# Kernel tuning notes

Hardware: AMD Instinct MI355X
Metric: run time of the kernel (lower is better)

Reference implementation:

```python
import jax, jax.numpy as jnp
import numpy as np
from jax import lax

B, C, HW = 8, 512, 32
NH = 8            # num_heads
NG = 32           # num_groups
HD = C // NH      # head_size = 64
EPS = 1e-6


def group_norm(x, gamma, beta, groups=NG, eps=EPS):
    b, c, h, w = x.shape
    xr = x.reshape(b, groups, c // groups, h, w)
    mu = xr.mean(axis=(2, 3, 4), keepdims=True)
    var = xr.var(axis=(2, 3, 4), keepdims=True)
    xn = ((xr - mu) / jnp.sqrt(var + eps)).reshape(b, c, h, w)
    return xn * gamma[None, :, None, None] + beta[None, :, None, None]


def conv2d(x, w, b):
    y = lax.conv_general_dilated(x, w, (1, 1), 'SAME',
                                 dimension_numbers=('NCHW', 'OIHW', 'NCHW'))
    return y + b[None, :, None, None]


def setup_inputs() -> dict:
    key = jax.random.key(0)
    ks = jax.random.split(key, 24)
    f32 = jnp.float32

    def lin(k, out_d, in_d):
        return (jax.random.normal(k, (out_d, in_d), f32) / np.sqrt(in_d)).astype(f32)

    inp = {
        'hidden_states': jax.random.normal(ks[0], (B, C, HW, HW), f32),
        'pre_g': jnp.ones(C, f32), 'pre_b': jnp.zeros(C, f32),
        'norm_g': jnp.ones(C, f32), 'norm_b': jnp.zeros(C, f32),
        'post_g': jnp.ones(C, f32), 'post_b': jnp.zeros(C, f32),
        'pos_emb': jax.random.normal(ks[1], (1, C, 32, 32), f32) * 0.02,
        'sa_w1': (jax.random.normal(ks[2], (C // 8, C, 1, 1), f32) / np.sqrt(C)),
        'sa_b1': jnp.zeros(C // 8, f32),
        'sa_w2': (jax.random.normal(ks[3], (C // 8, C // 8, 3, 3), f32) / np.sqrt(9 * C // 8)),
        'sa_b2': jnp.zeros(C // 8, f32),
        'sa_w3': (jax.random.normal(ks[4], (1, C // 8, 1, 1), f32) / np.sqrt(C // 8)),
        'sa_b3': jnp.zeros(1, f32),
        'wq': lin(ks[5], C, C), 'wk': lin(ks[6], C, C), 'wv': lin(ks[7], C, C),
        'wq0': lin(ks[8], C // 2, C), 'wk0': lin(ks[9], C // 2, C), 'wv0': lin(ks[10], C // 2, C),
        'wq1': lin(ks[11], C // 2, C), 'wk1': lin(ks[12], C // 2, C), 'wv1': lin(ks[13], C // 2, C),
        'ff_w1': lin(ks[14], C, 2 * C), 'ff_b1': jnp.zeros(C, f32),
        'ff_w2': lin(ks[15], C, C), 'ff_b2': jnp.zeros(C, f32),
        'out_w': lin(ks[16], C, C), 'out_b': jnp.zeros(C, f32),
    }
    return inp


def reference(hidden_states, pre_g, pre_b, norm_g, norm_b, post_g, post_b,
              pos_emb, sa_w1, sa_b1, sa_w2, sa_b2, sa_w3, sa_b3,
              wq, wk, wv, wq0, wk0, wv0, wq1, wk1, wv1,
              ff_w1, ff_b1, ff_w2, ff_b2, out_w, out_b):
    b, c, h, w = hidden_states.shape
    S = h * w
    residual = hidden_states

    hs = group_norm(hidden_states, pre_g, pre_b)
    # H=W=32 matches pos_embedding; bilinear resize to same size is identity
    hs = hs + pos_emb

    # spatial attention gating (conv 1x1 -> SiLU -> conv 3x3 -> SiLU -> conv 1x1 -> sigmoid)
    a = jax.nn.silu(conv2d(hs, sa_w1, sa_b1))
    a = jax.nn.silu(conv2d(a, sa_w2, sa_b2))
    spatial_weights = jax.nn.sigmoid(conv2d(a, sa_w3, sa_b3))
    spatial_enhanced = hs * spatial_weights

    # standard multi-head self-attention over flattened tokens
    sh = group_norm(hs, norm_g, norm_b).reshape(b, c, S).transpose(0, 2, 1)  # (B,S,C)
    ehs = sh  # encoder_hidden_states defaults to standard_hidden

    q = (sh @ wq.T).reshape(b, S, NH, HD)
    k = (ehs @ wk.T).reshape(b, S, NH, HD)
    v = (ehs @ wv.T).reshape(b, S, NH, HD)
    scores = jnp.einsum('bqhd,bkhd->bhqk', q, k) / np.sqrt(HD)
    probs = jax.nn.softmax(scores, axis=-1)
    std_out = jnp.einsum('bhqk,bkhd->bqhd', probs, v).reshape(b, S, c)

    # two multi-scale single-head attention branches (dim C/2 each)
    msh = spatial_enhanced.reshape(b, c, S).transpose(0, 2, 1)  # (B,S,C)
    parts = []
    for wqm, wkm, wvm in ((wq0, wk0, wv0), (wq1, wk1, wv1)):
        qm = msh @ wqm.T          # (B,S,C/2)
        km = ehs @ wkm.T
        vm = ehs @ wvm.T
        sc = jnp.einsum('bqd,bkd->bqk', qm, km) / np.sqrt(c // 2)
        parts.append(jnp.einsum('bqk,bkd->bqd', jax.nn.softmax(sc, axis=-1), vm))
    multi_out = jnp.concatenate(parts, axis=-1)  # (B,S,C)

    combined = jnp.concatenate([std_out, multi_out], axis=-1)  # (B,S,2C)
    fused = jax.nn.silu(combined @ ff_w1.T + ff_b1) @ ff_w2.T + ff_b2  # dropout = eval identity
    final = fused @ out_w.T + out_b
    final = final.transpose(0, 2, 1).reshape(b, c, h, w)
    final = group_norm(final, post_g, post_b)
    return final + residual
```

## Files before the change

kernel.cpp:

```cpp
#include <hip/hip_runtime.h>
#include <hip/hip_bf16.h>
#include <math.h>

typedef __attribute__((ext_vector_type(8))) __bf16 v8bf;
typedef __attribute__((ext_vector_type(4))) float v4f;

__device__ __forceinline__ unsigned short f2bf(float f) {
  union { float f; unsigned int u; } a; a.f = f;
  unsigned int r = a.u + 0x7fffu + ((a.u >> 16) & 1u);
  return (unsigned short)(r >> 16);
}
__device__ __forceinline__ unsigned short f2bf_trunc(float f) {
  union { float f; unsigned int u; } a; a.f = f;
  return (unsigned short)(a.u >> 16);
}
__device__ __forceinline__ float bf2f(unsigned short u) {
  union { unsigned int i; float f; } a; a.i = ((unsigned int)u) << 16; return a.f;
}
__device__ __forceinline__ float sigm(float x) { return 1.0f / (1.0f + __expf(-x)); }

__device__ __forceinline__ void async16(const void* g, void* l) {
  __builtin_amdgcn_global_load_lds(
      (const __attribute__((address_space(1))) unsigned int*)g,
      (__attribute__((address_space(3))) unsigned int*)l, 16, 0, 0);
}

__global__ __launch_bounds__(256) void gn_pre_kernel(
    const float* __restrict__ x, const float* __restrict__ g, const float* __restrict__ be,
    const float* __restrict__ pos, unsigned short* __restrict__ hsb, float* __restrict__ stats) {
  __shared__ float L[16384];
  __shared__ float rs[4], rs2[4], mr[2];
  int b = blockIdx.x >> 5, grp = blockIdx.x & 31;
  const float4* base = (const float4*)(x + ((size_t)b*512 + grp*16)*1024);
  float4* L4 = (float4*)L;
  int w = threadIdx.x >> 6;
  float s = 0.f, s2 = 0.f;
  for (int i = threadIdx.x; i < 4096; i += 256) {
    float4 v = base[i];
    L4[i] = v;
    s += v.x + v.y + v.z + v.w;
    s2 += v.x*v.x + v.y*v.y + v.z*v.z + v.w*v.w;
  }
#pragma unroll
  for (int o = 32; o; o >>= 1) { s += __shfl_xor(s, o); s2 += __shfl_xor(s2, o); }
  if ((threadIdx.x & 63) == 0) { rs[w] = s; rs2[w] = s2; }
  __syncthreads();
  if (threadIdx.x == 0) {
    float ts = rs[0]+rs[1]+rs[2]+rs[3], ts2 = rs2[0]+rs2[1]+rs2[2]+rs2[3];
    float mu = ts * (1.0f/16384.0f);
    float var = ts2 * (1.0f/16384.0f) - mu*mu;
    mr[0] = mu; mr[1] = rsqrtf(var + 1e-6f);
  }
  __syncthreads();
  float mu = mr[0], rstd = mr[1];
  const float4* pb = (const float4*)(pos + (size_t)grp*16*1024);
  float ns = 0.f, ns2 = 0.f;
  for (int i = threadIdx.x; i < 4096; i += 256) {
    float4 v = L4[i], p = pb[i];
    int c = grp*16 + (i >> 8);
    float gg = g[c], bb = be[c];
    float4 o;
    o.x = (v.x - mu)*rstd*gg + bb + p.x;
    o.y = (v.y - mu)*rstd*gg + bb + p.y;
    o.z = (v.z - mu)*rstd*gg + bb + p.z;
    o.w = (v.w - mu)*rstd*gg + bb + p.w;
    L4[i] = o;
    ns += o.x + o.y + o.z + o.w;
    ns2 += o.x*o.x + o.y*o.y + o.z*o.z + o.w*o.w;
  }
#pragma unroll
  for (int o = 32; o; o >>= 1) { ns += __shfl_xor(ns, o); ns2 += __shfl_xor(ns2, o); }
  if ((threadIdx.x & 63) == 0) { rs[w] = ns; rs2[w] = ns2; }
  __syncthreads();
  if (threadIdx.x == 0) {
    float ts = rs[0]+rs[1]+rs[2]+rs[3], ts2 = rs2[0]+rs2[1]+rs2[2]+rs2[3];
    float nmu = ts * (1.0f/16384.0f);
    float nvar = ts2 * (1.0f/16384.0f) - nmu*nmu;
    stats[(b*32+grp)*2] = nmu; stats[(b*32+grp)*2+1] = rsqrtf(nvar + 1e-6f);
  }
#pragma unroll
  for (int j = 0; j < 4; ++j) {
    int sI = threadIdx.x + j*256;
    unsigned int wd[8];
#pragma unroll
    for (int c = 0; c < 8; ++c) {
      unsigned int lo = f2bf(L[(2*c)*1024 + sI]);
      unsigned int hi = f2bf(L[(2*c+1)*1024 + sI]);
      wd[c] = lo | (hi << 16);
    }
    size_t oo = (size_t)(b*1024 + sI)*512 + grp*16;
    *(uint4*)(hsb + oo)     = make_uint4(wd[0], wd[1], wd[2], wd[3]);
    *(uint4*)(hsb + oo + 8) = make_uint4(wd[4], wd[5], wd[6], wd[7]);
  }
}

__global__ __launch_bounds__(256) void im2col_kernel(
    const unsigned short* __restrict__ a1, unsigned short* __restrict__ im2) {
  int row0 = blockIdx.x * 8;
#pragma unroll
  for (int it = 0; it < 3; ++it) {
    int cc = it*256 + threadIdx.x;
    if (cc >= 576) break;
    int rl = cc / 72, rr = cc - rl*72;
    int tap = rr >> 3, ch8 = rr & 7;
    int row = row0 + rl;
    int bb = row >> 10, s = row & 1023;
    int y = s >> 5, xx0 = s & 31;
    int yy = y + tap/3 - 1, xx = xx0 + tap%3 - 1;
    ushort4 v0 = make_ushort4(0,0,0,0), v1 = make_ushort4(0,0,0,0);
    if ((unsigned)yy < 32u && (unsigned)xx < 32u) {
      const unsigned short* src = a1 + ((size_t)(bb*1024 + yy*32 + xx))*64 + ch8*8;
      v0 = *(const ushort4*)src; v1 = *(const ushort4*)(src + 4);
    }
    unsigned short* dst = im2 + (size_t)row*576 + tap*64 + ch8*8;
    *(ushort4*)dst = v0; *(ushort4*)(dst + 4) = v1;
  }
}

__global__ __launch_bounds__(256) void gate_norm_kernel(
    const unsigned short* __restrict__ hsb, const unsigned short* __restrict__ a2,
    const float* __restrict__ w3, const float* __restrict__ b3,
    const float* __restrict__ stats, const float* __restrict__ g,
    const float* __restrict__ be,
    unsigned short* __restrict__ sh, unsigned short* __restrict__ msh) {
  int b = blockIdx.y;
  int s = blockIdx.x * 4 + (threadIdx.x >> 6);
  int oct = threadIdx.x & 63;
  int c0 = oct * 8;
  int grp = c0 >> 4;
  float part = bf2f(a2[((size_t)(b*1024) + s)*64 + oct]) * w3[oct];
#pragma unroll
  for (int o = 32; o; o >>= 1) part += __shfl_xor(part, o);
  float wgt = sigm(part + b3[0]);
  float mu = stats[(b*32 + grp)*2], rstd = stats[(b*32 + grp)*2 + 1];
  size_t o = (size_t)(b*1024 + s)*512 + c0;
  ushort4 u0 = *(const ushort4*)(hsb + o), u1 = *(const ushort4*)(hsb + o + 4);
  unsigned short uu[8] = {u0.x,u0.y,u0.z,u0.w,u1.x,u1.y,u1.z,u1.w};
  unsigned short so[8], mo[8];
#pragma unroll
  for (int j = 0; j < 8; ++j) {
    float v = bf2f(uu[j]);
    so[j] = f2bf((v - mu)*rstd*g[c0+j] + be[c0+j]);
    mo[j] = f2bf(v * wgt);
  }
  *(ushort4*)(sh + o)     = make_ushort4(so[0], so[1], so[2], so[3]);
  *(ushort4*)(sh + o + 4) = make_ushort4(so[4], so[5], so[6], so[7]);
  *(ushort4*)(msh + o)     = make_ushort4(mo[0], mo[1], mo[2], mo[3]);
  *(ushort4*)(msh + o + 4) = make_ushort4(mo[4], mo[5], mo[6], mo[7]);
}

struct WCvt { const float* src; int dstOff; int n; float scale; };
struct WCvtArgs { WCvt w[15]; };
__global__ __launch_bounds__(256) void wconvert_kernel(WCvtArgs a, unsigned short* __restrict__ dst) {
  WCvt e = a.w[blockIdx.y];
  int i = blockIdx.x * 256 + threadIdx.x;
  if (i >= e.n) return;
  if (blockIdx.y == 13) {
    int oc = i / 576, r = i - oc*576;
    int tap = r >> 6, ic = r & 63;
    dst[e.dstOff + i] = f2bf(e.src[(oc*64 + ic)*9 + tap]);
  } else if (blockIdx.y == 14) {
    dst[e.dstOff + i] = f2bf(e.src[(i & 511)*512 + (i >> 9)]);
  } else {
    dst[e.dstOff + i] = f2bf(e.src[i] * e.scale);
  }
}

__global__ __launch_bounds__(256) void bias_fold_kernel(
    const float* __restrict__ ow, const float* __restrict__ b2,
    const float* __restrict__ ob, float* __restrict__ bc) {
  int n = blockIdx.x * 256 + threadIdx.x;
  float s = ob[n];
  const float* r = ow + (size_t)n * 512;
#pragma unroll 8
  for (int j = 0; j < 512; ++j) s += r[j] * b2[j];
  bc[n] = s;
}

__global__ __launch_bounds__(256) void transpose2_kernel(
    const unsigned short* __restrict__ qkvm,
    unsigned short* __restrict__ vtb, unsigned short* __restrict__ vmt) {
  __shared__ unsigned short t[64][65];
  int s0 = blockIdx.x * 64, c0 = blockIdx.y * 64;
  int z = blockIdx.z, b = z & 7;
  const unsigned short* in = qkvm + (z >= 8 ? 2048 : 1024);
  unsigned short* out = (z >= 8) ? vmt : vtb;
  int tx = threadIdx.x & 63, ty = threadIdx.x >> 6;
#pragma unroll
  for (int i = 0; i < 16; ++i) {
    int s = ty + i*4;
    t[s][tx] = in[((size_t)(b*1024 + s0 + s))*2560 + c0 + tx];
  }
  __syncthreads();
#pragma unroll
  for (int i = 0; i < 16; ++i) {
    int c = ty + i*4;
    out[((size_t)b*512 + c0 + c)*1024 + s0 + tx] = t[tx][c];
  }
}

struct GemmDesc {
  const unsigned short* A; const unsigned short* B; void* out; const float* bias;
  int M, N, K, lda, ldb, ldo, epi;
  long long Ay, Az, By, Bz, Oy, Oz;
};

template<int BM, int BN>
__global__ __launch_bounds__(256) void gemm_tile_kernel(GemmDesc d) {
  constexpr int WGM = (BN >= 128) ? 2 : 4;
  constexpr int WGN = 4 / WGM;
  constexpr int MT = BM / (16 * WGM);
  constexpr int NT = BN / (16 * WGN);
  constexpr int AIT = (BM * 4) / 256;
  constexpr int BIT = (BN * 4) / 256;
  __shared__ __align__(16) unsigned short As[BM * 32];
  __shared__ __align__(16) unsigned short Bs[BN * 32];

  int ntx = d.N / BN, mtx = d.M / BM;
  int bmt, bnt;
  if ((mtx & 7) == 0) {
    int xcd = blockIdx.x & 7, j = blockIdx.x >> 3;
    int mpx = mtx >> 3;
    bmt = xcd * mpx + (j % mpx);
    bnt = j / mpx;
  } else {
    bmt = blockIdx.x / ntx; bnt = blockIdx.x % ntx;
  }
  int bm0 = bmt * BM, bn0 = bnt * BN;
  const unsigned short* A = d.A + (long long)blockIdx.y * d.Ay
      + (long long)blockIdx.z * d.Az + (size_t)bm0 * d.lda;
  const unsigned short* B = d.B + (long long)blockIdx.y * d.By
      + (long long)blockIdx.z * d.Bz + (size_t)bn0 * d.ldb;
  int tid = threadIdx.x, lane = tid & 63, w = tid >> 6;
  int wm = (WGN == 2) ? (w >> 1) : w;
  int wn = (WGN == 2) ? (w & 1) : 0;
  int ln = lane & 15, qd = lane >> 4;

  v4f acc[MT][NT];
#pragma unroll
  for (int i = 0; i < MT; ++i)
#pragma unroll
    for (int j = 0; j < NT; ++j) acc[i][j] = (v4f){0.f, 0.f, 0.f, 0.f};

  int nks = d.K >> 5;
  for (int ks = 0; ks < nks; ++ks) {
    int kof = ks * 32;
#pragma unroll
    for (int it = 0; it < AIT; ++it) {
      int c = it * 256 + tid;
      async16(A + (size_t)(c >> 2) * d.lda + (c & 3) * 8 + kof,
              As + (it * 256 + w * 64) * 8);
    }
#pragma unroll
    for (int it = 0; it < BIT; ++it) {
      int c = it * 256 + tid;
      async16(B + (size_t)(c >> 2) * d.ldb + (c & 3) * 8 + kof,
              Bs + (it * 256 + w * 64) * 8);
    }
    __syncthreads();
    v8bf af[MT], bfr[NT];
#pragma unroll
    for (int i = 0; i < MT; ++i)
      af[i] = *(const v8bf*)(As + (wm * MT * 16 + i * 16 + ln) * 32 + qd * 8);
#pragma unroll
    for (int j = 0; j < NT; ++j)
      bfr[j] = *(const v8bf*)(Bs + (wn * NT * 16 + j * 16 + ln) * 32 + qd * 8);
#pragma unroll
    for (int i = 0; i < MT; ++i)
#pragma unroll
      for (int j = 0; j < NT; ++j)
        acc[i][j] = __builtin_amdgcn_mfma_f32_16x16x32_bf16(af[i], bfr[j], acc[i][j], 0, 0, 0);
    __syncthreads();
  }

  size_t obase = (size_t)((long long)blockIdx.y * d.Oy + (long long)blockIdx.z * d.Oz);
#pragma unroll
  for (int i = 0; i < MT; ++i) {
#pragma unroll
    for (int j = 0; j < NT; ++j) {
      int col = bn0 + wn * NT * 16 + j * 16 + ln;
      float bia = d.bias ? d.bias[col] : 0.0f;
#pragma unroll
      for (int r = 0; r < 4; ++r) {
        int row = bm0 + wm * MT * 16 + i * 16 + qd * 4 + r;
        float v = acc[i][j][r] + bia;
        if (d.epi == 2) v = v * sigm(v);
        size_t oi = obase + (size_t)row * d.ldo + col;
        if (d.epi == 0) ((float*)d.out)[oi] = v;
        else ((unsigned short*)d.out)[oi] = f2bf(v);
      }
    }
  }
}

__global__ __launch_bounds__(256) void flash_attn_kernel(
    const unsigned short* __restrict__ QKVM, const unsigned short* __restrict__ VTB,
    unsigned short* __restrict__ out) {
  __shared__ __align__(16) unsigned short Ks[128*64];
  __shared__ __align__(16) unsigned short Vts[64*128];
  __shared__ __align__(16) unsigned short Pw[4][16*128];
  int h = blockIdx.x, b = blockIdx.y, qt = blockIdx.z;
  int tid = threadIdx.x, lane = tid & 63, w = tid >> 6;
  int ln = lane & 15, qd = lane >> 4;

  const unsigned short* Qbase = QKVM + ((size_t)(b*1024 + qt*128 + w*32))*2560 + h*64;
  v8bf aq[2][2];
#pragma unroll
  for (int i = 0; i < 2; ++i)
#pragma unroll
    for (int s = 0; s < 2; ++s)
      aq[i][s] = *(const v8bf*)(Qbase + (size_t)(i*16 + ln)*2560 + s*32 + qd*8);

  v4f o_acc[2][4];
  float l_part[2][4];
#pragma unroll
  for (int i = 0; i < 2; ++i)
#pragma unroll
    for (int dn = 0; dn < 4; ++dn) o_acc[i][dn] = (v4f){0.f,0.f,0.f,0.f};
#pragma unroll
  for (int i = 0; i < 2; ++i)
#pragma unroll
    for (int r = 0; r < 4; ++r) l_part[i][r] = 0.f;

  const unsigned short* Kg = QKVM + 512 + (size_t)(b*1024)*2560 + h*64;
  const unsigned short* Vg = VTB + ((size_t)(b*512) + h*64)*1024;

  for (int kt = 0; kt < 8; ++kt) {
#pragma unroll
    for (int it = 0; it < 4; ++it) {
      int c = it*256 + tid;
      async16(Kg + (size_t)(kt*128 + (c >> 3))*2560 + (((c & 7) ^ ((c >> 3) & 7)) << 3),
              Ks + c*8);
    }
#pragma unroll
    for (int it = 0; it < 4; ++it) {
      int c = it*256 + tid;
      async16(Vg + (size_t)(c >> 4)*1024 + kt*128 + ((((c & 15) ^ ((c >> 4) & 7))) << 3),
              Vts + c*8);
    }
    __syncthreads();

#pragma unroll
    for (int i = 0; i < 2; ++i) {
      v4f sc[8];
#pragma unroll
      for (int n = 0; n < 8; ++n) {
        v4f a = (v4f){0.f,0.f,0.f,0.f};
#pragma unroll
        for (int s = 0; s < 2; ++s) {
          v8bf kb = *(const v8bf*)(Ks + (n*16 + ln)*64 + (((s*4 + qd) ^ (ln & 7)) << 3));
          a = __builtin_amdgcn_mfma_f32_16x16x32_bf16(aq[i][s], kb, a, 0, 0, 0);
        }
        sc[n] = a;
      }
#pragma unroll
      for (int r = 0; r < 4; ++r) {
        int row7 = (qd*4 + r) & 7;
        float acc_l = 0.f;
#pragma unroll
        for (int n = 0; n < 8; ++n) {
          float p = exp2f(sc[n][r]);
          acc_l += p;
          Pw[w][(qd*4 + r)*128 + (((n*2 + (ln >> 3)) ^ row7) << 3) + (ln & 7)] = f2bf_trunc(p);
        }
        l_part[i][r] += acc_l;
      }
#pragma unroll
      for (int dn = 0; dn < 4; ++dn) {
        v4f a = o_acc[i][dn];
#pragma unroll
        for (int ks2 = 0; ks2 < 4; ++ks2) {
          int phys = (((ks2*4 + qd) ^ (ln & 7)) << 3);
          v8bf pf = *(const v8bf*)(&Pw[w][ln*128 + phys]);
          v8bf vf = *(const v8bf*)(Vts + (dn*16 + ln)*128 + phys);
          a = __builtin_amdgcn_mfma_f32_16x16x32_bf16(pf, vf, a, 0, 0, 0);
        }
        o_acc[i][dn] = a;
      }
    }
    __syncthreads();
  }

  unsigned short* ob = out + ((size_t)(b*1024 + qt*128 + w*32))*1024 + h*64;
#pragma unroll
  for (int i = 0; i < 2; ++i)
#pragma unroll
    for (int r = 0; r < 4; ++r) {
      float l = l_part[i][r];
      l += __shfl_xor(l, 1); l += __shfl_xor(l, 2);
      l += __shfl_xor(l, 4); l += __shfl_xor(l, 8);
      float rinv = 1.0f / l;
#pragma unroll
      for (int dn = 0; dn < 4; ++dn)
        ob[(size_t)(i*16 + qd*4 + r)*1024 + dn*16 + ln] = f2bf(o_acc[i][dn][r] * rinv);
    }
}

__global__ __launch_bounds__(256) void softmax_bf16_kernel(
    const unsigned short* __restrict__ S, unsigned short* __restrict__ P, int nrows) {
  int row = blockIdx.x * 4 + (threadIdx.x >> 6);
  if (row >= nrows) return;
  int l = threadIdx.x & 63;
  const ushort4* sp = (const ushort4*)(S + (size_t)row * 1024);
  float v[16];
  float m = -1e30f;
#pragma unroll
  for (int t = 0; t < 4; ++t) {
    ushort4 u = sp[t*64 + l];
    v[t*4+0] = bf2f(u.x); v[t*4+1] = bf2f(u.y); v[t*4+2] = bf2f(u.z); v[t*4+3] = bf2f(u.w);
    m = fmaxf(m, fmaxf(fmaxf(v[t*4], v[t*4+1]), fmaxf(v[t*4+2], v[t*4+3])));
  }
#pragma unroll
  for (int o = 32; o; o >>= 1) m = fmaxf(m, __shfl_xor(m, o));
  float sum = 0.f;
#pragma unroll
  for (int t = 0; t < 16; ++t) { v[t] = __expf(v[t] - m); sum += v[t]; }
#pragma unroll
  for (int o = 32; o; o >>= 1) sum += __shfl_xor(sum, o);
  float r = 1.0f / sum;
  ushort4* p = (ushort4*)(P + (size_t)row * 1024);
#pragma unroll
  for (int t = 0; t < 4; ++t)
    p[t*64 + l] = make_ushort4(f2bf_trunc(v[t*4]*r), f2bf_trunc(v[t*4+1]*r),
                               f2bf_trunc(v[t*4+2]*r), f2bf_trunc(v[t*4+3]*r));
}

__global__ __launch_bounds__(256) void gn_stats_bf16_kernel(
    const unsigned short* __restrict__ t, float* __restrict__ stats) {
  int b = blockIdx.x >> 5, grp = blockIdx.x & 31;
  float s = 0.f, s2 = 0.f;
#pragma unroll
  for (int j = 0; j < 4; ++j) {
    int sI = threadIdx.x + j*256;
    const unsigned short* p = t + ((size_t)(b*1024 + sI))*512 + grp*16;
    uint4 a = *(const uint4*)p, c2 = *(const uint4*)(p + 8);
    unsigned int ww[8] = {a.x,a.y,a.z,a.w,c2.x,c2.y,c2.z,c2.w};
#pragma unroll
    for (int k = 0; k < 8; ++k) {
      float lo = bf2f((unsigned short)(ww[k] & 0xffff));
      float hi = bf2f((unsigned short)(ww[k] >> 16));
      s += lo + hi; s2 += lo*lo + hi*hi;
    }
  }
#pragma unroll
  for (int o = 32; o; o >>= 1) { s += __shfl_xor(s, o); s2 += __shfl_xor(s2, o); }
  __shared__ float rs[4], rs2[4];
  int w = threadIdx.x >> 6;
  if ((threadIdx.x & 63) == 0) { rs[w] = s; rs2[w] = s2; }
  __syncthreads();
  if (threadIdx.x == 0) {
    float ts = rs[0]+rs[1]+rs[2]+rs[3], ts2 = rs2[0]+rs2[1]+rs2[2]+rs2[3];
    float mu = ts * (1.0f/16384.0f);
    float var = ts2 * (1.0f/16384.0f) - mu*mu;
    stats[(b*32+grp)*2] = mu; stats[(b*32+grp)*2+1] = rsqrtf(var + 1e-6f);
  }
}

__global__ __launch_bounds__(256) void final_out_kernel(
    const unsigned short* __restrict__ fin, const float* __restrict__ stats,
    const float* __restrict__ g, const float* __restrict__ be,
    const float* __restrict__ x, float* __restrict__ out) {
  __shared__ float t[64][65];
  int s0 = blockIdx.x * 64, c0 = blockIdx.y * 64, b = blockIdx.z;
  int tx = threadIdx.x & 63, ty = threadIdx.x >> 6;
#pragma unroll
  for (int i = 0; i < 16; ++i) {
    int s = ty + i*4;
    t[s][tx] = bf2f(fin[((size_t)(b*1024 + s0 + s))*512 + c0 + tx]);
  }
  __syncthreads();
#pragma unroll
  for (int i = 0; i < 16; ++i) {
    int c = ty + i*4;
    int cc = c0 + c, grp = cc >> 4;
    float mu = stats[(b*32+grp)*2], rstd = stats[(b*32+grp)*2+1];
    float gg = g[cc], bb = be[cc];
    size_t oi = ((size_t)(b*512 + cc))*1024 + s0 + tx;
    out[oi] = (t[tx][c] - mu)*rstd*gg + bb + x[oi];
  }
}

static void launch_gemm128(hipStream_t st, const unsigned short* A, const unsigned short* B,
                           void* out, const float* bias,
                           int M, int N, int K, int lda, int ldb, int ldo, int epi,
                           long long Ay, long long Az, long long By, long long Bz,
                           long long Oy, long long Oz, int gy, int gz) {
  GemmDesc d{A, B, out, bias, M, N, K, lda, ldb, ldo, epi, Ay, Az, By, Bz, Oy, Oz};
  gemm_tile_kernel<128,128><<<dim3((M/128)*(N/128), gy, gz), dim3(256), 0, st>>>(d);
}
static void launch_gemm64(hipStream_t st, const unsigned short* A, const unsigned short* B,
                          void* out, const float* bias,
                          int M, int N, int K, int lda, int ldb, int ldo, int epi) {
  GemmDesc d{A, B, out, bias, M, N, K, lda, ldb, ldo, epi, 0,0,0,0,0,0};
  gemm_tile_kernel<128,64><<<dim3((M/128)*(N/64), 1, 1), dim3(256), 0, st>>>(d);
}

extern "C" void kernel_launch(void* const* d_in, const int* in_sizes, int n_in,
                              void* d_out, int out_size, void* d_ws, size_t ws_size,
                              hipStream_t stream) {
  const float* x      = (const float*)d_in[0];
  const float* pre_g  = (const float*)d_in[1];
  const float* pre_b  = (const float*)d_in[2];
  const float* norm_g = (const float*)d_in[3];
  const float* norm_b = (const float*)d_in[4];
  const float* post_g = (const float*)d_in[5];
  const float* post_b = (const float*)d_in[6];
  const float* pos    = (const float*)d_in[7];
  const float* sa_b1  = (const float*)d_in[9];
  const float* sa_b2  = (const float*)d_in[11];
  const float* sa_w3  = (const float*)d_in[12];
  const float* sa_b3  = (const float*)d_in[13];
  const float* ff_b1  = (const float*)d_in[24];
  const float* ff_b2  = (const float*)d_in[26];
  const float* out_w  = (const float*)d_in[27];
  const float* out_b  = (const float*)d_in[28];
  float* outp = (float*)d_out;

  char* ws = (char*)d_ws;
  size_t off = 0;
  auto alloc = [&](size_t bytes) -> void* {
    void* p = ws + off; off += (bytes + 255) & ~(size_t)255; return p;
  };
  float* STATS = (float*)alloc(4096);
  float* BC    = (float*)alloc(2048);
  unsigned short* HSB  = (unsigned short*)alloc(8388608);
  unsigned short* A1   = (unsigned short*)alloc(1048576);
  unsigned short* IM2  = (unsigned short*)alloc(9437184);
  unsigned short* A2   = (unsigned short*)alloc(1048576);
  unsigned short* SHB  = (unsigned short*)alloc(8388608);
  unsigned short* MSHB = (unsigned short*)alloc(8388608);
  unsigned short* WBF  = (unsigned short*)alloc(6291456);
  unsigned short* WCOMB= (unsigned short*)alloc(524288);
  unsigned short* QKVM = (unsigned short*)alloc(41943040);
  unsigned short* QM   = (unsigned short*)alloc(8388608);
  unsigned short* VTB  = (unsigned short*)alloc(8388608);
  unsigned short* VMT  = (unsigned short*)alloc(8388608);
  unsigned short* SBUF = (unsigned short*)alloc(33554432);
  unsigned short* PBUF = (unsigned short*)alloc(33554432);
  unsigned short* COMB = (unsigned short*)alloc(16777216);
  unsigned short* FFMID= (unsigned short*)alloc(8388608);
  unsigned short* FINALB=(unsigned short*)alloc(8388608);

  const int OQKVM=0, OQM=1310720, OFF1=1572864, OFF2T=2097152,
            OOW=2359296, OW1=2621440, OW2R=2654208;

  gn_pre_kernel<<<dim3(256), dim3(256), 0, stream>>>(x, pre_g, pre_b, pos, HSB, STATS);
  {
    WCvtArgs a;
    const float LG2E = 1.4426950408889634f;
    const int   srcIdx[15] = {14,15,16, 18,21,19,22, 17,20, 23,27, 8, 0 , 10, 25};
    const int   dofs[15]   = {0, 262144, 524288,
                              786432, 917504, 1048576, 1179648,
                              OQM, OQM+131072,
                              OFF1, OOW, OW1, 0, OW2R, OFF2T};
    const int   ns[15]     = {262144,262144,262144, 131072,131072,131072,131072,
                              131072,131072, 524288,262144, 32768, 0, 36864, 262144};
    const float sc[15]     = {0.125f*LG2E,1.f,1.f, 1.f,1.f,1.f,1.f,
                              0.0625f,0.0625f, 1.f,1.f, 1.f, 0.f, 1.f, 1.f};
    for (int i = 0; i < 15; ++i) { a.w[i].src = (const float*)d_in[srcIdx[i]]; a.w[i].dstOff = dofs[i]; a.w[i].n = ns[i]; a.w[i].scale = sc[i]; }
    wconvert_kernel<<<dim3(2048, 15), dim3(256), 0, stream>>>(a, WBF);
  }
  {
    GemmDesc d{WBF+OOW, WBF+OFF2T, WCOMB, nullptr, 512, 512, 512, 512, 512, 512, 1, 0,0,0,0,0,0};
    gemm_tile_kernel<128,128><<<dim3(16, 1, 1), dim3(256), 0, stream>>>(d);
  }
  bias_fold_kernel<<<dim3(2), dim3(256), 0, stream>>>(out_w, ff_b2, out_b, BC);
  launch_gemm64(stream, HSB, WBF+OW1,  A1, sa_b1, 8192, 64, 512, 512, 512, 64, 2);
  im2col_kernel<<<dim3(1024), dim3(256), 0, stream>>>(A1, IM2);
  launch_gemm64(stream, IM2, WBF+OW2R, A2, sa_b2, 8192, 64, 576, 576, 576, 64, 2);
  gate_norm_kernel<<<dim3(256, 8), dim3(256), 0, stream>>>(HSB, A2, sa_w3, sa_b3, STATS, norm_g, norm_b, SHB, MSHB);

  launch_gemm128(stream, SHB,  WBF+OQKVM, QKVM, nullptr, 8192, 2560, 512, 512, 512, 2560, 1, 0,0,0,0,0,0, 1,1);
  launch_gemm128(stream, MSHB, WBF+OQM,   QM,   nullptr, 8192, 512,  512, 512, 512, 512,  1, 0,0,0,0,0,0, 1,1);

  transpose2_kernel<<<dim3(16, 8, 16), dim3(256), 0, stream>>>(QKVM, VTB, VMT);

  flash_attn_kernel<<<dim3(8, 8, 8), dim3(256), 0, stream>>>(QKVM, VTB, COMB);

  launch_gemm128(stream, QM, QKVM + 1536, SBUF, nullptr,
                 1024, 1024, 256, 512, 2560, 1024, 1,
                 1024LL*512, 256, 1024LL*2560, 256, 1024LL*1024, 8388608, 8, 2);
  softmax_bf16_kernel<<<dim3(4096), dim3(256), 0, stream>>>(SBUF, PBUF, 16384);
  launch_gemm128(stream, PBUF, VMT, COMB + 512, nullptr,
                 1024, 256, 1024, 1024, 1024, 1024, 1,
                 1024LL*1024, 8388608, 512LL*1024, 256LL*1024, 1024LL*1024, 256, 8, 2);

  launch_gemm128(stream, COMB,  WBF+OFF1, FFMID,  ff_b1, 8192, 512, 1024, 1024, 1024, 512, 2, 0,0,0,0,0,0, 1,1);
  launch_gemm128(stream, FFMID, WCOMB,    FINALB, BC,    8192, 512, 512,  512,  512,  512, 1, 0,0,0,0,0,0, 1,1);

  gn_stats_bf16_kernel<<<dim3(256), dim3(256), 0, stream>>>(FINALB, STATS);
  final_out_kernel<<<dim3(16, 8, 8), dim3(256), 0, stream>>>(FINALB, STATS, post_g, post_b, x, outp);

  (void)in_sizes; (void)n_in; (void)out_size; (void)ws_size;
}
```

Measured before the change: 457.3 us.

## Deepen GEMM K-tile with swizzled LDS, widen flash-attn blocks, use smaller GEMM tiles

The generic GEMM now stages a 64-wide K slice per iteration with an XOR-swizzled LDS layout. This halves the barriers per K step and is meant to cut LDS bank conflicts, at the cost of twice the shared memory per block. Flash attention moves to 512-thread blocks, each wave holding 16 query rows instead of 32, so K/V tiles in LDS are shared across more waves and per-wave register use drops. Three N=512 GEMMs switch to the 64-wide tile launcher to put more blocks on the GPU.

```diff
diff --git a/kernel.cpp b/kernel.cpp
--- a/kernel.cpp
+++ b/kernel.cpp
@@ -211,10 +211,10 @@
   constexpr int WGN = 4 / WGM;
   constexpr int MT = BM / (16 * WGM);
   constexpr int NT = BN / (16 * WGN);
-  constexpr int AIT = (BM * 4) / 256;
-  constexpr int BIT = (BN * 4) / 256;
-  __shared__ __align__(16) unsigned short As[BM * 32];
-  __shared__ __align__(16) unsigned short Bs[BN * 32];
+  constexpr int AIT = (BM * 8) / 256;
+  constexpr int BIT = (BN * 8) / 256;
+  __shared__ __align__(16) unsigned short As[BM * 64];
+  __shared__ __align__(16) unsigned short Bs[BN * 64];
 
   int ntx = d.N / BN, mtx = d.M / BM;
   int bmt, bnt;
@@ -242,34 +242,41 @@
 #pragma unroll
     for (int j = 0; j < NT; ++j) acc[i][j] = (v4f){0.f, 0.f, 0.f, 0.f};
 
-  int nks = d.K >> 5;
+  int nks = d.K >> 6;
   for (int ks = 0; ks < nks; ++ks) {
-    int kof = ks * 32;
+    int kof = ks * 64;
 #pragma unroll
     for (int it = 0; it < AIT; ++it) {
       int c = it * 256 + tid;
-      async16(A + (size_t)(c >> 2) * d.lda + (c & 3) * 8 + kof,
-              As + (it * 256 + w * 64) * 8);
+      int row = c >> 3, ch = c & 7;
+      async16(A + (size_t)row * d.lda + ((ch ^ (row & 7)) << 3) + kof, As + c * 8);
     }
 #pragma unroll
     for (int it = 0; it < BIT; ++it) {
       int c = it * 256 + tid;
-      async16(B + (size_t)(c >> 2) * d.ldb + (c & 3) * 8 + kof,
-              Bs + (it * 256 + w * 64) * 8);
+      int row = c >> 3, ch = c & 7;
+      async16(B + (size_t)row * d.ldb + ((ch ^ (row & 7)) << 3) + kof, Bs + c * 8);
     }
     __syncthreads();
-    v8bf af[MT], bfr[NT];
-#pragma unroll
-    for (int i = 0; i < MT; ++i)
-      af[i] = *(const v8bf*)(As + (wm * MT * 16 + i * 16 + ln) * 32 + qd * 8);
-#pragma unroll
-    for (int j = 0; j < NT; ++j)
-      bfr[j] = *(const v8bf*)(Bs + (wn * NT * 16 + j * 16 + ln) * 32 + qd * 8);
-#pragma unroll
-    for (int i = 0; i < MT; ++i)
-#pragma unroll
-      for (int j = 0; j < NT; ++j)
-        acc[i][j] = __builtin_amdgcn_mfma_f32_16x16x32_bf16(af[i], bfr[j], acc[i][j], 0, 0, 0);
+#pragma unroll
+    for (int k2 = 0; k2 < 2; ++k2) {
+      v8bf af[MT], bfr[NT];
+#pragma unroll
+      for (int i = 0; i < MT; ++i) {
+        int row = wm * MT * 16 + i * 16 + ln;
+        af[i] = *(const v8bf*)(As + row * 64 + (((k2*4 + qd) ^ (ln & 7)) << 3));
+      }
+#pragma unroll
+      for (int j = 0; j < NT; ++j) {
+        int row = wn * NT * 16 + j * 16 + ln;
+        bfr[j] = *(const v8bf*)(Bs + row * 64 + (((k2*4 + qd) ^ (ln & 7)) << 3));
+      }
+#pragma unroll
+      for (int i = 0; i < MT; ++i)
+#pragma unroll
+        for (int j = 0; j < NT; ++j)
+          acc[i][j] = __builtin_amdgcn_mfma_f32_16x16x32_bf16(af[i], bfr[j], acc[i][j], 0, 0, 0);
+    }
     __syncthreads();
   }
 
@@ -293,107 +300,96 @@
   }
 }
 
-__global__ __launch_bounds__(256) void flash_attn_kernel(
+__global__ __launch_bounds__(512) void flash_attn_kernel(
     const unsigned short* __restrict__ QKVM, const unsigned short* __restrict__ VTB,
     unsigned short* __restrict__ out) {
   __shared__ __align__(16) unsigned short Ks[128*64];
   __shared__ __align__(16) unsigned short Vts[64*128];
-  __shared__ __align__(16) unsigned short Pw[4][16*128];
+  __shared__ __align__(16) unsigned short Pw[8][16*128];
   int h = blockIdx.x, b = blockIdx.y, qt = blockIdx.z;
   int tid = threadIdx.x, lane = tid & 63, w = tid >> 6;
   int ln = lane & 15, qd = lane >> 4;
 
-  const unsigned short* Qbase = QKVM + ((size_t)(b*1024 + qt*128 + w*32))*2560 + h*64;
-  v8bf aq[2][2];
-#pragma unroll
-  for (int i = 0; i < 2; ++i)
-#pragma unroll
-    for (int s = 0; s < 2; ++s)
-      aq[i][s] = *(const v8bf*)(Qbase + (size_t)(i*16 + ln)*2560 + s*32 + qd*8);
-
-  v4f o_acc[2][4];
-  float l_part[2][4];
-#pragma unroll
-  for (int i = 0; i < 2; ++i)
-#pragma unroll
-    for (int dn = 0; dn < 4; ++dn) o_acc[i][dn] = (v4f){0.f,0.f,0.f,0.f};
-#pragma unroll
-  for (int i = 0; i < 2; ++i)
-#pragma unroll
-    for (int r = 0; r < 4; ++r) l_part[i][r] = 0.f;
+  const unsigned short* Qbase = QKVM + ((size_t)(b*1024 + qt*128 + w*16))*2560 + h*64;
+  v8bf aq[2];
+#pragma unroll
+  for (int s = 0; s < 2; ++s)
+    aq[s] = *(const v8bf*)(Qbase + (size_t)ln*2560 + s*32 + qd*8);
+
+  v4f o_acc[4];
+  float l_part[4];
+#pragma unroll
+  for (int dn = 0; dn < 4; ++dn) o_acc[dn] = (v4f){0.f,0.f,0.f,0.f};
+#pragma unroll
+  for (int r = 0; r < 4; ++r) l_part[r] = 0.f;
 
   const unsigned short* Kg = QKVM + 512 + (size_t)(b*1024)*2560 + h*64;
   const unsigned short* Vg = VTB + ((size_t)(b*512) + h*64)*1024;
 
   for (int kt = 0; kt < 8; ++kt) {
 #pragma unroll
-    for (int it = 0; it < 4; ++it) {
-      int c = it*256 + tid;
+    for (int it = 0; it < 2; ++it) {
+      int c = it*512 + tid;
       async16(Kg + (size_t)(kt*128 + (c >> 3))*2560 + (((c & 7) ^ ((c >> 3) & 7)) << 3),
               Ks + c*8);
     }
 #pragma unroll
-    for (int it = 0; it < 4; ++it) {
-      int c = it*256 + tid;
+    for (int it = 0; it < 2; ++it) {
+      int c = it*512 + tid;
       async16(Vg + (size_t)(c >> 4)*1024 + kt*128 + ((((c & 15) ^ ((c >> 4) & 7))) << 3),
               Vts + c*8);
     }
     __syncthreads();
 
-#pragma unroll
-    for (int i = 0; i < 2; ++i) {
-      v4f sc[8];
+    v4f sc[8];
+#pragma unroll
+    for (int n = 0; n < 8; ++n) {
+      v4f a = (v4f){0.f,0.f,0.f,0.f};
+#pragma unroll
+      for (int s = 0; s < 2; ++s) {
+        v8bf kb = *(const v8bf*)(Ks + (n*16 + ln)*64 + (((s*4 + qd) ^ (ln & 7)) << 3));
+        a = __builtin_amdgcn_mfma_f32_16x16x32_bf16(aq[s], kb, a, 0, 0, 0);
+      }
+      sc[n] = a;
+    }
+#pragma unroll
+    for (int r = 0; r < 4; ++r) {
+      int row7 = (qd*4 + r) & 7;
+      float acc_l = 0.f;
 #pragma unroll
       for (int n = 0; n < 8; ++n) {
-        v4f a = (v4f){0.f,0.f,0.f,0.f};
-#pragma unroll
-        for (int s = 0; s < 2; ++s) {
-          v8bf kb = *(const v8bf*)(Ks + (n*16 + ln)*64 + (((s*4 + qd) ^ (ln & 7)) << 3));
-          a = __builtin_amdgcn_mfma_f32_16x16x32_bf16(aq[i][s], kb, a, 0, 0, 0);
-        }
-        sc[n] = a;
+        float p = exp2f(sc[n][r]);
+        acc_l += p;
+        Pw[w][(qd*4 + r)*128 + (((n*2 + (ln >> 3)) ^ row7) << 3) + (ln & 7)] = f2bf_trunc(p);
       }
-#pragma unroll
-      for (int r = 0; r < 4; ++r) {
-        int row7 = (qd*4 + r) & 7;
-        float acc_l = 0.f;
-#pragma unroll
-        for (int n = 0; n < 8; ++n) {
-          float p = exp2f(sc[n][r]);
-          acc_l += p;
-          Pw[w][(qd*4 + r)*128 + (((n*2 + (ln >> 3)) ^ row7) << 3) + (ln & 7)] = f2bf_trunc(p);
-        }
-        l_part[i][r] += acc_l;
+      l_part[r] += acc_l;
+    }
+#pragma unroll
+    for (int dn = 0; dn < 4; ++dn) {
+      v4f a = o_acc[dn];
+#pragma unroll
+      for (int ks2 = 0; ks2 < 4; ++ks2) {
+        int phys = (((ks2*4 + qd) ^ (ln & 7)) << 3);
+        v8bf pf = *(const v8bf*)(&Pw[w][ln*128 + phys]);
+        v8bf vf = *(const v8bf*)(Vts + (dn*16 + ln)*128 + phys);
+        a = __builtin_amdgcn_mfma_f32_16x16x32_bf16(pf, vf, a, 0, 0, 0);
       }
-#pragma unroll
-      for (int dn = 0; dn < 4; ++dn) {
-        v4f a = o_acc[i][dn];
-#pragma unroll
-        for (int ks2 = 0; ks2 < 4; ++ks2) {
-          int phys = (((ks2*4 + qd) ^ (ln & 7)) << 3);
-          v8bf pf = *(const v8bf*)(&Pw[w][ln*128 + phys]);
-          v8bf vf = *(const v8bf*)(Vts + (dn*16 + ln)*128 + phys);
-          a = __builtin_amdgcn_mfma_f32_16x16x32_bf16(pf, vf, a, 0, 0, 0);
-        }
-        o_acc[i][dn] = a;
-      }
+      o_acc[dn] = a;
     }
     __syncthreads();
   }
 
-  unsigned short* ob = out + ((size_t)(b*1024 + qt*128 + w*32))*1024 + h*64;
-#pragma unroll
-  for (int i = 0; i < 2; ++i)
-#pragma unroll
-    for (int r = 0; r < 4; ++r) {
-      float l = l_part[i][r];
-      l += __shfl_xor(l, 1); l += __shfl_xor(l, 2);
-      l += __shfl_xor(l, 4); l += __shfl_xor(l, 8);
-      float rinv = 1.0f / l;
-#pragma unroll
-      for (int dn = 0; dn < 4; ++dn)
-        ob[(size_t)(i*16 + qd*4 + r)*1024 + dn*16 + ln] = f2bf(o_acc[i][dn][r] * rinv);
-    }
+  unsigned short* ob = out + ((size_t)(b*1024 + qt*128 + w*16))*1024 + h*64;
+#pragma unroll
+  for (int r = 0; r < 4; ++r) {
+    float l = l_part[r];
+    l += __shfl_xor(l, 1); l += __shfl_xor(l, 2);
+    l += __shfl_xor(l, 4); l += __shfl_xor(l, 8);
+    float rinv = 1.0f / l;
+#pragma unroll
+    for (int dn = 0; dn < 4; ++dn)
+      ob[(size_t)(qd*4 + r)*1024 + dn*16 + ln] = f2bf(o_acc[dn][r] * rinv);
+  }
 }
 
 __global__ __launch_bounds__(256) void softmax_bf16_kernel(
@@ -548,7 +544,7 @@
   {
     WCvtArgs a;
     const float LG2E = 1.4426950408889634f;
-    const int   srcIdx[15] = {14,15,16, 18,21,19,22, 17,20, 23,27, 8, 0 , 10, 25};
+    const int   srcIdx[15] = {14,15,16, 18,21,19,22, 17,20, 23,27, 8, 0, 10, 25};
     const int   dofs[15]   = {0, 262144, 524288,
                               786432, 917504, 1048576, 1179648,
                               OQM, OQM+131072,
@@ -571,11 +567,11 @@
   gate_norm_kernel<<<dim3(256, 8), dim3(256), 0, stream>>>(HSB, A2, sa_w3, sa_b3, STATS, norm_g, norm_b, SHB, MSHB);
 
   launch_gemm128(stream, SHB,  WBF+OQKVM, QKVM, nullptr, 8192, 2560, 512, 512, 512, 2560, 1, 0,0,0,0,0,0, 1,1);
-  launch_gemm128(stream, MSHB, WBF+OQM,   QM,   nullptr, 8192, 512,  512, 512, 512, 512,  1, 0,0,0,0,0,0, 1,1);
+  launch_gemm64(stream, MSHB, WBF+OQM,   QM,   nullptr, 8192, 512,  512, 512, 512, 512,  1);
 
   transpose2_kernel<<<dim3(16, 8, 16), dim3(256), 0, stream>>>(QKVM, VTB, VMT);
 
-  flash_attn_kernel<<<dim3(8, 8, 8), dim3(256), 0, stream>>>(QKVM, VTB, COMB);
+  flash_attn_kernel<<<dim3(8, 8, 8), dim3(512), 0, stream>>>(QKVM, VTB, COMB);
 
   launch_gemm128(stream, QM, QKVM + 1536, SBUF, nullptr,
                  1024, 1024, 256, 512, 2560, 1024, 1,
@@ -585,8 +581,8 @@
                  1024, 256, 1024, 1024, 1024, 1024, 1,
                  1024LL*1024, 8388608, 512LL*1024, 256LL*1024, 1024LL*1024, 256, 8, 2);
 
-  launch_gemm128(stream, COMB,  WBF+OFF1, FFMID,  ff_b1, 8192, 512, 1024, 1024, 1024, 512, 2, 0,0,0,0,0,0, 1,1);
-  launch_gemm128(stream, FFMID, WCOMB,    FINALB, BC,    8192, 512, 512,  512,  512,  512, 1, 0,0,0,0,0,0, 1,1);
+  launch_gemm64(stream, COMB,  WBF+OFF1, FFMID,  ff_b1, 8192, 512, 1024, 1024, 1024, 512, 2);
+  launch_gemm64(stream, FFMID, WCOMB,    FINALB, BC,    8192, 512, 512,  512,  512,  512, 1);
 
   gn_stats_bf16_kernel<<<dim3(256), dim3(256), 0, stream>>>(FINALB, STATS);
   final_out_kernel<<<dim3(16, 8, 8), dim3(256), 0, stream>>>(FINALB, STATS, post_g, post_b, x, outp);
```

New measurement: 406.7 us. 11.1% less time.
